# Optimization experiments

Hardware: AMD Instinct MI355X
Metric: run time of the kernel (lower is better)

Reference implementation:

```python
import jax, jax.numpy as jnp
import numpy as np

VOCAB, EMB, H, LAYERS, B, T = 50000, 128, 128, 3, 64, 512


def _lstm_dir(x, w_ih, w_hh, b_ih, b_hh, h0, c0, reverse):
    # x: [B,T,Din]; w_ih: [4H,Din]; w_hh: [4H,H]; h0,c0: [B,H]
    xg = jnp.einsum('btd,gd->btg', x, w_ih) + b_ih + b_hh  # [B,T,4H]

    def step(carry, xg_t):
        h, c = carry
        g = xg_t + h @ w_hh.T  # [B,4H]
        i, f, gg, o = jnp.split(g, 4, axis=-1)  # torch gate order i,f,g,o
        c = jax.nn.sigmoid(f) * c + jax.nn.sigmoid(i) * jnp.tanh(gg)
        h = jax.nn.sigmoid(o) * jnp.tanh(c)
        return (h, c), h

    _, hs = jax.lax.scan(step, (h0, c0), jnp.swapaxes(xg, 0, 1), reverse=reverse)
    return jnp.swapaxes(hs, 0, 1)  # [B,T,H], aligned with input time order


def _bidir_layer(x, w_ih, w_hh, b_ih, b_hh, h0, c0):
    # stacked params: leading dim 2 = (fwd, bwd)
    fwd = _lstm_dir(x, w_ih[0], w_hh[0], b_ih[0], b_hh[0], h0[0], c0[0], False)
    bwd = _lstm_dir(x, w_ih[1], w_hh[1], b_ih[1], b_hh[1], h0[1], c0[1], True)
    return jnp.concatenate([fwd, bwd], axis=-1)  # [B,T,2H]


def setup_inputs() -> dict:
    key = jax.random.key(0)
    ks = jax.random.split(key, 20)
    s = 1.0 / np.sqrt(H)
    inp = {
        'X_batch': jax.random.randint(ks[0], (B, T), 0, VOCAB),
        'emb': jax.random.normal(ks[1], (VOCAB, EMB), jnp.float32),
        'hx': jax.random.normal(ks[2], (2 * LAYERS, B, H), jnp.float32),
        'cx': jax.random.normal(ks[3], (2 * LAYERS, B, H), jnp.float32),
        'lin_w': jax.random.uniform(ks[4], (1, 2 * H), jnp.float32, -s, s),
        'lin_b': jax.random.uniform(ks[5], (1,), jnp.float32, -s, s),
    }
    k = 6
    for l in range(LAYERS):
        din = EMB if l == 0 else 2 * H
        inp[f'w_ih_{l}'] = jax.random.uniform(ks[k], (2, 4 * H, din), jnp.float32, -s, s); k += 1
        inp[f'w_hh_{l}'] = jax.random.uniform(ks[k], (2, 4 * H, H), jnp.float32, -s, s); k += 1
        inp[f'b_ih_{l}'] = jax.random.uniform(ks[k], (2, 4 * H), jnp.float32, -s, s); k += 1
        inp[f'b_hh_{l}'] = jax.random.uniform(ks[k], (2, 4 * H), jnp.float32, -s, s); k += 1
    return inp


def reference(X_batch, emb, hx, cx, lin_w, lin_b,
              w_ih_0, w_hh_0, b_ih_0, b_hh_0,
              w_ih_1, w_hh_1, b_ih_1, b_hh_1,
              w_ih_2, w_hh_2, b_ih_2, b_hh_2):
    x = emb[X_batch]  # [B,T,EMB]
    params = [(w_ih_0, w_hh_0, b_ih_0, b_hh_0),
              (w_ih_1, w_hh_1, b_ih_1, b_hh_1),
              (w_ih_2, w_hh_2, b_ih_2, b_hh_2)]
    for l, (wi, wh, bi, bh) in enumerate(params):
        x = _bidir_layer(x, wi, wh, bi, bh, hx[2 * l:2 * l + 2], cx[2 * l:2 * l + 2])
    # linear head applied to last timestep (== output[:, -1] of full linear)
    return x[:, -1] @ lin_w.T + lin_b  # [B,1]
```

## Files before the change

kernel.cpp:

```cpp
#include <hip/hip_runtime.h>
#include <hip/hip_bf16.h>
#include <stdint.h>

#define B_    64
#define T_    512
#define EMB_  128
#define H_    128
#define G4    512
#define M_    (B_ * T_)

typedef __attribute__((ext_vector_type(8))) short     short8;
typedef __attribute__((ext_vector_type(4))) float     floatx4;
typedef __attribute__((ext_vector_type(2))) _Float16  half2v;

#define GLDS(g, l) __builtin_amdgcn_global_load_lds( \
    (__attribute__((address_space(1))) void*)(g),    \
    (__attribute__((address_space(3))) void*)(l), 16, 0, 0)

__device__ __forceinline__ unsigned short f2bf_bits(float f) {
  __hip_bfloat16 h = __float2bfloat16(f);
  return *reinterpret_cast<unsigned short*>(&h);
}
__device__ __forceinline__ float bf_bits2f(unsigned short u) {
  unsigned int x = ((unsigned int)u) << 16;
  return __uint_as_float(x);
}
__device__ __forceinline__ float sigm(float x) {
  return __fdividef(1.0f, 1.0f + __expf(-x));
}
__device__ __forceinline__ float tanh_fast(float x) {
  return 1.0f - __fdividef(2.0f, __expf(2.0f * x) + 1.0f);
}

__device__ __forceinline__ unsigned int pack_f16x2(float a, float b) {
  half2v h; h.x = (_Float16)a; h.y = (_Float16)b;
  return __builtin_bit_cast(unsigned int, h);
}
__device__ __forceinline__ half2v u2h2(unsigned int u) {
  return __builtin_bit_cast(half2v, u);
}

#if __has_builtin(__builtin_amdgcn_fdot2)
__device__ __forceinline__ float fdot2(half2v a, half2v b, float c) {
  return __builtin_amdgcn_fdot2(a, b, c, false);
}
#else
__device__ __forceinline__ float fdot2(half2v a, half2v b, float c) {
  return fmaf((float)a.x, (float)b.x, fmaf((float)a.y, (float)b.y, c));
}
#endif

__device__ __forceinline__ float quad_sum(float x) {
  x += __int_as_float(
      __builtin_amdgcn_mov_dpp(__float_as_int(x), 0xB1, 0xF, 0xF, true));
  x += __int_as_float(
      __builtin_amdgcn_mov_dpp(__float_as_int(x), 0x4E, 0xF, 0xF, true));
  return x;
}

__device__ __forceinline__ void barrier_lds_only() {
  __builtin_amdgcn_s_waitcnt(0xC07F);
  __builtin_amdgcn_s_barrier();
}

__device__ __forceinline__ void  store_xg(float* p, float v)  { *p = v; }
__device__ __forceinline__ void  store_xg(unsigned short* p, float v) { *p = f2bf_bits(v); }
__device__ __forceinline__ float load_xg(const float* p)  { return *p; }
__device__ __forceinline__ float load_xg(const unsigned short* p) { return bf_bits2f(*p); }

__global__ void k_gather(const int* __restrict__ X, const float* __restrict__ emb,
                         unsigned short* __restrict__ x0) {
  int i = blockIdx.x * 256 + threadIdx.x;
  int row = i >> 5, c4 = i & 31;
  float4 v = ((const float4*)emb)[(size_t)X[row] * 32 + c4];
  ushort4 o;
  o.x = f2bf_bits(v.x); o.y = f2bf_bits(v.y); o.z = f2bf_bits(v.z); o.w = f2bf_bits(v.w);
  ((ushort4*)x0)[i] = o;
}

__global__ void k_prep(const float* __restrict__ w, const float* __restrict__ bi,
                       const float* __restrict__ bh, unsigned short* __restrict__ wb,
                       float* __restrict__ bias, int nw) {
  int i = blockIdx.x * blockDim.x + threadIdx.x;
  int stride = gridDim.x * blockDim.x;
  for (int k = i; k < nw; k += stride) wb[k] = f2bf_bits(w[k]);
  for (int k = i; k < 2 * G4; k += stride) bias[k] = bi[k] + bh[k];
}

__global__ void k_prep_whh(const float* __restrict__ Whh, unsigned int* __restrict__ wf) {
  int i = blockIdx.x * 256 + threadIdx.x;
  int dir   = i >> 15;
  int r     = i & 0x7FFF;
  int plane = r >> 9;
  int ts    = r & 511;
  int g = plane >> 4;
  int j = plane & 15;
  int l = ts & 63, w = ts >> 6;
  int p2 = l & 3, ul = l >> 2;
  int u  = w * 16 + ul;
  int k0 = 32 * p2 + 2 * j;
  const float* wr = Whh + ((size_t)dir * G4 + g * H_ + u) * H_ + k0;
  wf[i] = pack_f16x2(wr[0], wr[1]);
}

template <typename XG_T>
__global__ __launch_bounds__(256, 2) void k_gemm(
    const unsigned short* __restrict__ A,
    const unsigned short* __restrict__ W,
    const float* __restrict__ bias,
    XG_T* __restrict__ xg,
    int K) {
  __shared__ unsigned short sA[128 * 32];
  __shared__ unsigned short sB[128 * 32];
  const int tid  = threadIdx.x;
  const int lane = tid & 63;
  const int wave = tid >> 6;
  const int mt = blockIdx.x, nt = blockIdx.y, dir = blockIdx.z;
  const size_t Arow0 = (size_t)mt * 128;
  const int    Ncol0 = nt * 128;
  const unsigned short* Wd = W + (size_t)dir * G4 * K;

  const int srow = tid >> 2;
  const int qlog = (tid & 3) ^ ((tid >> 4) & 3);
  auto ldsA0 = (__attribute__((address_space(3))) void*)(sA + wave * 512);
  auto ldsA1 = (__attribute__((address_space(3))) void*)(sA + 2048 + wave * 512);
  auto ldsB0 = (__attribute__((address_space(3))) void*)(sB + wave * 512);
  auto ldsB1 = (__attribute__((address_space(3))) void*)(sB + 2048 + wave * 512);

  floatx4 acc[4][4];
#pragma unroll
  for (int i = 0; i < 4; ++i)
#pragma unroll
    for (int j = 0; j < 4; ++j) acc[i][j] = (floatx4)0.0f;

  const int wrow = (wave >> 1) * 64, wcol = (wave & 1) * 64;
  const int frow = lane & 15;
  const int fq   = lane >> 4;

  for (int kt = 0; kt < K; kt += 32) {
    const unsigned short* gA0 = A  + (Arow0 + srow) * (size_t)K + kt + qlog * 8;
    const unsigned short* gB0 = Wd + (size_t)(Ncol0 + srow) * K + kt + qlog * 8;
    GLDS(gA0, ldsA0);
    GLDS(gA0 + (size_t)64 * K, ldsA1);
    GLDS(gB0, ldsB0);
    GLDS(gB0 + (size_t)64 * K, ldsB1);
    __syncthreads();

    short8 af[4], bf[4];
#pragma unroll
    for (int i = 0; i < 4; ++i) {
      int r  = wrow + 16 * i + frow;
      int rn = wcol + 16 * i + frow;
      af[i] = *(const short8*)(sA + r  * 32 + ((fq ^ ((r  >> 2) & 3)) * 8));
      bf[i] = *(const short8*)(sB + rn * 32 + ((fq ^ ((rn >> 2) & 3)) * 8));
    }
#pragma unroll
    for (int i = 0; i < 4; ++i)
#pragma unroll
      for (int j = 0; j < 4; ++j)
        acc[i][j] = __builtin_amdgcn_mfma_f32_16x16x32_bf16(af[i], bf[j], acc[i][j], 0, 0, 0);
    __syncthreads();
  }

  const int r0 = (lane >> 4) * 4;
  const int cc = lane & 15;
  XG_T* xgd = xg + (size_t)dir * M_ * G4;
#pragma unroll
  for (int j = 0; j < 4; ++j) {
    int gcol = Ncol0 + wcol + 16 * j + cc;
    float bs = bias[dir * G4 + gcol];
#pragma unroll
    for (int i = 0; i < 4; ++i) {
      size_t rowb = Arow0 + wrow + 16 * i + r0;
#pragma unroll
      for (int r = 0; r < 4; ++r)
        store_xg(&xgd[(rowb + r) * G4 + gcol], acc[i][j][r] + bs);
    }
  }
}

template <typename XG_T>
__global__ __attribute__((amdgpu_flat_work_group_size(512, 512),
                          amdgpu_waves_per_eu(2, 2))) void k_scan(
    const unsigned int* __restrict__ wf,
    const float* __restrict__ hx0,
    const float* __restrict__ cx0,
    const XG_T* __restrict__ xg,
    unsigned short* __restrict__ y)
{
  const int b   = blockIdx.x & 63;
  const int dir = blockIdx.x >> 6;
  const int tid = threadIdx.x;
  const int lane = tid & 63;
  const int wave = tid >> 6;
  const int p2 = lane & 3;
  const int ul = lane >> 2;
  const int u  = wave * 16 + ul;

  __shared__ __align__(16) unsigned short h16[2][128];

  unsigned int wvs[64];
#pragma unroll
  for (int i = 0; i < 64; ++i) wvs[i] = wf[((dir * 64 + i) << 9) + tid];

  float c = cx0[(size_t)dir * B_ * H_ + b * H_ + u];
  if (p2 == 0) {
    float h0 = hx0[(size_t)dir * B_ * H_ + b * H_ + u];
    h16[0][u] = (unsigned short)(pack_f16x2(h0, 0.0f) & 0xFFFF);
  }

  const XG_T* xgb = xg + ((size_t)dir * M_ + (size_t)b * T_) * G4;
  const intptr_t xstep = dir ? -(intptr_t)G4 : (intptr_t)G4;
  const int o0 = p2 * H_ + u;
  const XG_T* xrow0 = xgb + (dir ? (size_t)(T_ - 1) * G4 : 0);
  float xa0 = load_xg(xrow0 + o0);
  float xa1 = load_xg(xrow0 + xstep + o0);
  const XG_T* xld = xrow0 + 2 * xstep;

  unsigned short* yp = y + ((size_t)b * T_ + (dir ? T_ - 1 : 0)) * (2 * H_)
                         + dir * H_ + u;
  const intptr_t ystep = dir ? -(intptr_t)(2 * H_) : (intptr_t)(2 * H_);

  __syncthreads();

  auto step = [&](int par, float xv) {
    const char* hb = (const char*)&h16[par][0] + 64 * p2;
    uint4 hq[4];
#pragma unroll
    for (int i = 0; i < 4; ++i) hq[i] = *(const uint4*)(hb + 16 * i);
    unsigned int hhd[16];
#pragma unroll
    for (int i = 0; i < 4; ++i) {
      hhd[4 * i + 0] = hq[i].x; hhd[4 * i + 1] = hq[i].y;
      hhd[4 * i + 2] = hq[i].z; hhd[4 * i + 3] = hq[i].w;
    }
    float A0 = (p2 == 0) ? xv : 0.0f, B0 = 0;
    float A1 = (p2 == 1) ? xv : 0.0f, B1 = 0;
    float A2 = (p2 == 2) ? xv : 0.0f, B2 = 0;
    float A3 = (p2 == 3) ? xv : 0.0f, B3 = 0;
#pragma unroll
    for (int j = 0; j < 8; ++j) {
      int j1 = j + 8;
      A0 = fdot2(u2h2(wvs[0 * 16 + j]),  u2h2(hhd[j]),  A0);
      A1 = fdot2(u2h2(wvs[1 * 16 + j]),  u2h2(hhd[j]),  A1);
      A2 = fdot2(u2h2(wvs[2 * 16 + j]),  u2h2(hhd[j]),  A2);
      A3 = fdot2(u2h2(wvs[3 * 16 + j]),  u2h2(hhd[j]),  A3);
      B0 = fdot2(u2h2(wvs[0 * 16 + j1]), u2h2(hhd[j1]), B0);
      B1 = fdot2(u2h2(wvs[1 * 16 + j1]), u2h2(hhd[j1]), B1);
      B2 = fdot2(u2h2(wvs[2 * 16 + j1]), u2h2(hhd[j1]), B2);
      B3 = fdot2(u2h2(wvs[3 * 16 + j1]), u2h2(hhd[j1]), B3);
    }
    float g0 = quad_sum(A0 + B0);
    float g1 = quad_sum(A1 + B1);
    float g2 = quad_sum(A2 + B2);
    float g3 = quad_sum(A3 + B3);
    float iv = sigm(g0), fv = sigm(g1), gv = tanh_fast(g2), ov = sigm(g3);
    c = fmaf(fv, c, iv * gv);
    float h = ov * tanh_fast(c);
    if (p2 == 0) {
      h16[par ^ 1][u] = (unsigned short)(pack_f16x2(h, 0.0f) & 0xFFFF);
      *yp = f2bf_bits(h);
    }
    yp += ystep;
    barrier_lds_only();
  };

  for (int t = 0; t < T_; t += 2) {
    {
      float xv = xa0;
      xa0 = load_xg(xld + o0);
      xld += xstep;
      step(0, xv);
    }
    {
      float xv = xa1;
      xa1 = load_xg(xld + o0);
      xld += xstep;
      step(1, xv);
    }
  }
}

__global__ void k_head(const unsigned short* __restrict__ y2, const float* __restrict__ lw,
                       const float* __restrict__ lb, float* __restrict__ out) {
  int b = blockIdx.x, l = threadIdx.x;
  const unsigned short* row = y2 + ((size_t)b * T_ + (T_ - 1)) * (2 * H_);
  float s = 0;
#pragma unroll
  for (int k = 0; k < 4; ++k) s += bf_bits2f(row[l + 64 * k]) * lw[l + 64 * k];
#pragma unroll
  for (int off = 32; off > 0; off >>= 1) s += __shfl_down(s, off);
  if (l == 0) out[b] = s + lb[0];
}

template <typename XG_T>
static inline void run_layers(const unsigned int* const* wfs,
                              const unsigned short* x0,
                              unsigned short* y0, unsigned short* y1, unsigned short* y2,
                              const unsigned short* wb0, const unsigned short* wb1,
                              const unsigned short* wb2,
                              const float* bias0, const float* bias1, const float* bias2,
                              const float* hx, const float* cx,
                              XG_T* xg, hipStream_t stream) {
  dim3 gg(M_ / 128, G4 / 128, 2);
  k_gemm<XG_T><<<gg, 256, 0, stream>>>(x0, wb0, bias0, xg, EMB_);
  k_scan<XG_T><<<128, 512, 0, stream>>>(wfs[0], hx, cx, xg, y0);
  k_gemm<XG_T><<<gg, 256, 0, stream>>>(y0, wb1, bias1, xg, 2 * H_);
  k_scan<XG_T><<<128, 512, 0, stream>>>(wfs[1], hx + 2 * B_ * H_, cx + 2 * B_ * H_, xg, y1);
  k_gemm<XG_T><<<gg, 256, 0, stream>>>(y1, wb2, bias2, xg, 2 * H_);
  k_scan<XG_T><<<128, 512, 0, stream>>>(wfs[2], hx + 4 * B_ * H_, cx + 4 * B_ * H_, xg, y2);
}

extern "C" void kernel_launch(void* const* d_in, const int* in_sizes, int n_in,
                              void* d_out, int out_size, void* d_ws, size_t ws_size,
                              hipStream_t stream) {
  const int*   X   = (const int*)d_in[0];
  const float* emb = (const float*)d_in[1];
  const float* hx  = (const float*)d_in[2];
  const float* cx  = (const float*)d_in[3];
  const float* lw  = (const float*)d_in[4];
  const float* lb  = (const float*)d_in[5];
  const float* w_ih[3] = {(const float*)d_in[6],  (const float*)d_in[10], (const float*)d_in[14]};
  const float* w_hh[3] = {(const float*)d_in[7],  (const float*)d_in[11], (const float*)d_in[15]};
  const float* b_ih[3] = {(const float*)d_in[8],  (const float*)d_in[12], (const float*)d_in[16]};
  const float* b_hh[3] = {(const float*)d_in[9],  (const float*)d_in[13], (const float*)d_in[17]};
  float* out = (float*)d_out;

  char* ws = (char*)d_ws;
  size_t off = 0;
  auto carve = [&](size_t bytes) {
    char* p = ws + off;
    off = (off + bytes + 255) & ~(size_t)255;
    return p;
  };
  unsigned short* x0  = (unsigned short*)carve((size_t)M_ * EMB_ * 2);
  unsigned short* y0  = (unsigned short*)carve((size_t)M_ * 2 * H_ * 2);
  unsigned short* y1  = (unsigned short*)carve((size_t)M_ * 2 * H_ * 2);
  unsigned short* y2  = (unsigned short*)carve((size_t)M_ * 2 * H_ * 2);
  unsigned short* wb0 = (unsigned short*)carve((size_t)2 * G4 * EMB_ * 2);
  unsigned short* wb1 = (unsigned short*)carve((size_t)2 * G4 * 2 * H_ * 2);
  unsigned short* wb2 = (unsigned short*)carve((size_t)2 * G4 * 2 * H_ * 2);
  float* bias0 = (float*)carve(2 * G4 * 4);
  float* bias1 = (float*)carve(2 * G4 * 4);
  float* bias2 = (float*)carve(2 * G4 * 4);
  unsigned int* wf0 = (unsigned int*)carve((size_t)65536 * 4);
  unsigned int* wf1 = (unsigned int*)carve((size_t)65536 * 4);
  unsigned int* wf2 = (unsigned int*)carve((size_t)65536 * 4);
  const size_t xg_f32_bytes = (size_t)2 * M_ * G4 * 4;
  const bool use_f32 = (off + xg_f32_bytes) <= ws_size;
  void* xg = carve(use_f32 ? xg_f32_bytes : xg_f32_bytes / 2);

  k_prep<<<256, 256, 0, stream>>>(w_ih[0], b_ih[0], b_hh[0], wb0, bias0, 2 * G4 * EMB_);
  k_prep<<<256, 256, 0, stream>>>(w_ih[1], b_ih[1], b_hh[1], wb1, bias1, 2 * G4 * 2 * H_);
  k_prep<<<256, 256, 0, stream>>>(w_ih[2], b_ih[2], b_hh[2], wb2, bias2, 2 * G4 * 2 * H_);
  k_prep_whh<<<256, 256, 0, stream>>>(w_hh[0], wf0);
  k_prep_whh<<<256, 256, 0, stream>>>(w_hh[1], wf1);
  k_prep_whh<<<256, 256, 0, stream>>>(w_hh[2], wf2);
  k_gather<<<(M_ * 32) / 256, 256, 0, stream>>>(X, emb, x0);

  const unsigned int* wfs[3] = {wf0, wf1, wf2};
  if (use_f32)
    run_layers<float>(wfs, x0, y0, y1, y2, wb0, wb1, wb2, bias0, bias1, bias2,
                      hx, cx, (float*)xg, stream);
  else
    run_layers<unsigned short>(wfs, x0, y0, y1, y2, wb0, wb1, wb2, bias0, bias1, bias2,
                               hx, cx, (unsigned short*)xg, stream);

  k_head<<<64, 64, 0, stream>>>(y2, lw, lb, out);
}
```

Before: 1.370 ms.

## Compute LSTM recurrent matvec with MFMA instead of fdot2 in scan kernel

Replaces the per-step fdot2-based recurrent matvec (512 threads, quad DPP reduction) with 16x16x32 f16 MFMA instructions over 256 threads. Each wave holds W_hh fragments as MFMA B operands, and only row 0 of the A operand carries h, so 15 of 16 rows are wasted. The W_hh prep layout is rewritten to match. The aim is to cut the serial per-step latency of the recurrence by dropping the dot-product chain and cross-lane reductions, at the cost of MFMA latency and wasted matrix rows.

```diff
diff --git a/kernel.cpp b/kernel.cpp
--- a/kernel.cpp
+++ b/kernel.cpp
@@ -12,6 +12,7 @@
 typedef __attribute__((ext_vector_type(8))) short     short8;
 typedef __attribute__((ext_vector_type(4))) float     floatx4;
 typedef __attribute__((ext_vector_type(2))) _Float16  half2v;
+typedef __attribute__((ext_vector_type(8))) _Float16  half8;
 
 #define GLDS(g, l) __builtin_amdgcn_global_load_lds( \
     (__attribute__((address_space(1))) void*)(g),    \
@@ -31,31 +32,9 @@
 __device__ __forceinline__ float tanh_fast(float x) {
   return 1.0f - __fdividef(2.0f, __expf(2.0f * x) + 1.0f);
 }
-
 __device__ __forceinline__ unsigned int pack_f16x2(float a, float b) {
   half2v h; h.x = (_Float16)a; h.y = (_Float16)b;
   return __builtin_bit_cast(unsigned int, h);
-}
-__device__ __forceinline__ half2v u2h2(unsigned int u) {
-  return __builtin_bit_cast(half2v, u);
-}
-
-#if __has_builtin(__builtin_amdgcn_fdot2)
-__device__ __forceinline__ float fdot2(half2v a, half2v b, float c) {
-  return __builtin_amdgcn_fdot2(a, b, c, false);
-}
-#else
-__device__ __forceinline__ float fdot2(half2v a, half2v b, float c) {
-  return fmaf((float)a.x, (float)b.x, fmaf((float)a.y, (float)b.y, c));
-}
-#endif
-
-__device__ __forceinline__ float quad_sum(float x) {
-  x += __int_as_float(
-      __builtin_amdgcn_mov_dpp(__float_as_int(x), 0xB1, 0xF, 0xF, true));
-  x += __int_as_float(
-      __builtin_amdgcn_mov_dpp(__float_as_int(x), 0x4E, 0xF, 0xF, true));
-  return x;
 }
 
 __device__ __forceinline__ void barrier_lds_only() {
@@ -89,17 +68,17 @@
 
 __global__ void k_prep_whh(const float* __restrict__ Whh, unsigned int* __restrict__ wf) {
   int i = blockIdx.x * 256 + threadIdx.x;
-  int dir   = i >> 15;
-  int r     = i & 0x7FFF;
-  int plane = r >> 9;
-  int ts    = r & 511;
-  int g = plane >> 4;
-  int j = plane & 15;
-  int l = ts & 63, w = ts >> 6;
-  int p2 = l & 3, ul = l >> 2;
-  int u  = w * 16 + ul;
-  int k0 = 32 * p2 + 2 * j;
-  const float* wr = Whh + ((size_t)dir * G4 + g * H_ + u) * H_ + k0;
+  int jp  = i & 3;
+  int l   = (i >> 2) & 63;
+  int kk  = (i >> 8) & 3;
+  int uh  = (i >> 10) & 1;
+  int g   = (i >> 11) & 3;
+  int w   = (i >> 13) & 3;
+  int dir = (i >> 15) & 1;
+  int u   = w * 32 + uh * 16 + (l & 15);
+  int row = g * 128 + u;
+  int k0  = kk * 32 + (l >> 4) * 8 + 2 * jp;
+  const float* wr = Whh + ((size_t)dir * G4 + row) * H_ + k0;
   wf[i] = pack_f16x2(wr[0], wr[1]);
 }
 
@@ -180,8 +159,8 @@
 }
 
 template <typename XG_T>
-__global__ __attribute__((amdgpu_flat_work_group_size(512, 512),
-                          amdgpu_waves_per_eu(2, 2))) void k_scan(
+__global__ __attribute__((amdgpu_flat_work_group_size(256, 256),
+                          amdgpu_waves_per_eu(1, 1))) void k_scan(
     const unsigned int* __restrict__ wf,
     const float* __restrict__ hx0,
     const float* __restrict__ cx0,
@@ -192,92 +171,119 @@
   const int dir = blockIdx.x >> 6;
   const int tid = threadIdx.x;
   const int lane = tid & 63;
-  const int wave = tid >> 6;
-  const int p2 = lane & 3;
-  const int ul = lane >> 2;
-  const int u  = wave * 16 + ul;
+  const int w    = tid >> 6;
+  const int l15  = lane & 15;
+  const int seg  = lane >> 4;
+  const bool row0 = (l15 == 0);
 
   __shared__ __align__(16) unsigned short h16[2][128];
 
-  unsigned int wvs[64];
-#pragma unroll
-  for (int i = 0; i < 64; ++i) wvs[i] = wf[((dir * 64 + i) << 9) + tid];
-
-  float c = cx0[(size_t)dir * B_ * H_ + b * H_ + u];
-  if (p2 == 0) {
-    float h0 = hx0[(size_t)dir * B_ * H_ + b * H_ + u];
-    h16[0][u] = (unsigned short)(pack_f16x2(h0, 0.0f) & 0xFFFF);
-  }
+  half8 wB[4][2][4];
+  {
+    const uint4* wv4 = (const uint4*)wf;
+#pragma unroll
+    for (int g = 0; g < 4; ++g)
+#pragma unroll
+      for (int uh = 0; uh < 2; ++uh)
+#pragma unroll
+        for (int kk = 0; kk < 4; ++kk) {
+          int idx = ((((dir * 4 + w) * 4 + g) * 2 + uh) * 4 + kk) * 64 + lane;
+          wB[g][uh][kk] = __builtin_bit_cast(half8, wv4[idx]);
+        }
+  }
+
+  float c[2];
+#pragma unroll
+  for (int uh = 0; uh < 2; ++uh)
+    c[uh] = cx0[(size_t)dir * B_ * H_ + b * H_ + (w * 32 + uh * 16 + l15)];
+
+  if (tid < 128) {
+    float h0 = hx0[(size_t)dir * B_ * H_ + b * H_ + tid];
+    h16[0][tid] = (unsigned short)(pack_f16x2(h0, 0.0f) & 0xFFFF);
+  }
+
+  floatx4 acc[4][2];
+#pragma unroll
+  for (int g = 0; g < 4; ++g)
+#pragma unroll
+    for (int uh = 0; uh < 2; ++uh) acc[g][uh] = (floatx4)0.0f;
 
   const XG_T* xgb = xg + ((size_t)dir * M_ + (size_t)b * T_) * G4;
   const intptr_t xstep = dir ? -(intptr_t)G4 : (intptr_t)G4;
-  const int o0 = p2 * H_ + u;
+  int xofs[4][2];
+#pragma unroll
+  for (int g = 0; g < 4; ++g)
+#pragma unroll
+    for (int uh = 0; uh < 2; ++uh)
+      xofs[g][uh] = g * H_ + w * 32 + uh * 16 + l15;
   const XG_T* xrow0 = xgb + (dir ? (size_t)(T_ - 1) * G4 : 0);
-  float xa0 = load_xg(xrow0 + o0);
-  float xa1 = load_xg(xrow0 + xstep + o0);
+  float xpA[4][2], xpB[4][2];
+#pragma unroll
+  for (int g = 0; g < 4; ++g)
+#pragma unroll
+    for (int uh = 0; uh < 2; ++uh) {
+      xpA[g][uh] = load_xg(xrow0 + xofs[g][uh]);
+      xpB[g][uh] = load_xg(xrow0 + xstep + xofs[g][uh]);
+    }
   const XG_T* xld = xrow0 + 2 * xstep;
 
   unsigned short* yp = y + ((size_t)b * T_ + (dir ? T_ - 1 : 0)) * (2 * H_)
-                         + dir * H_ + u;
+                         + dir * H_;
   const intptr_t ystep = dir ? -(intptr_t)(2 * H_) : (intptr_t)(2 * H_);
 
   __syncthreads();
 
-  auto step = [&](int par, float xv) {
-    const char* hb = (const char*)&h16[par][0] + 64 * p2;
-    uint4 hq[4];
-#pragma unroll
-    for (int i = 0; i < 4; ++i) hq[i] = *(const uint4*)(hb + 16 * i);
-    unsigned int hhd[16];
-#pragma unroll
-    for (int i = 0; i < 4; ++i) {
-      hhd[4 * i + 0] = hq[i].x; hhd[4 * i + 1] = hq[i].y;
-      hhd[4 * i + 2] = hq[i].z; hhd[4 * i + 3] = hq[i].w;
-    }
-    float A0 = (p2 == 0) ? xv : 0.0f, B0 = 0;
-    float A1 = (p2 == 1) ? xv : 0.0f, B1 = 0;
-    float A2 = (p2 == 2) ? xv : 0.0f, B2 = 0;
-    float A3 = (p2 == 3) ? xv : 0.0f, B3 = 0;
-#pragma unroll
-    for (int j = 0; j < 8; ++j) {
-      int j1 = j + 8;
-      A0 = fdot2(u2h2(wvs[0 * 16 + j]),  u2h2(hhd[j]),  A0);
-      A1 = fdot2(u2h2(wvs[1 * 16 + j]),  u2h2(hhd[j]),  A1);
-      A2 = fdot2(u2h2(wvs[2 * 16 + j]),  u2h2(hhd[j]),  A2);
-      A3 = fdot2(u2h2(wvs[3 * 16 + j]),  u2h2(hhd[j]),  A3);
-      B0 = fdot2(u2h2(wvs[0 * 16 + j1]), u2h2(hhd[j1]), B0);
-      B1 = fdot2(u2h2(wvs[1 * 16 + j1]), u2h2(hhd[j1]), B1);
-      B2 = fdot2(u2h2(wvs[2 * 16 + j1]), u2h2(hhd[j1]), B2);
-      B3 = fdot2(u2h2(wvs[3 * 16 + j1]), u2h2(hhd[j1]), B3);
-    }
-    float g0 = quad_sum(A0 + B0);
-    float g1 = quad_sum(A1 + B1);
-    float g2 = quad_sum(A2 + B2);
-    float g3 = quad_sum(A3 + B3);
-    float iv = sigm(g0), fv = sigm(g1), gv = tanh_fast(g2), ov = sigm(g3);
-    c = fmaf(fv, c, iv * gv);
-    float h = ov * tanh_fast(c);
-    if (p2 == 0) {
-      h16[par ^ 1][u] = (unsigned short)(pack_f16x2(h, 0.0f) & 0xFFFF);
-      *yp = f2bf_bits(h);
+  auto step = [&](int par, float (&xp)[4][2]) {
+    half8 af[4];
+#pragma unroll
+    for (int kk = 0; kk < 4; ++kk) {
+      uint4 hv = *(const uint4*)((const char*)&h16[par][0] + kk * 64 + seg * 16);
+      uint4 av;
+      av.x = row0 ? hv.x : 0u; av.y = row0 ? hv.y : 0u;
+      av.z = row0 ? hv.z : 0u; av.w = row0 ? hv.w : 0u;
+      af[kk] = __builtin_bit_cast(half8, av);
+    }
+
+#pragma unroll
+    for (int g = 0; g < 4; ++g)
+#pragma unroll
+      for (int uh = 0; uh < 2; ++uh) {
+        acc[g][uh][0] = xp[g][uh];
+        xp[g][uh] = load_xg(xld + xofs[g][uh]);
+      }
+    xld += xstep;
+
+#pragma unroll
+    for (int kk = 0; kk < 4; ++kk)
+#pragma unroll
+      for (int g = 0; g < 4; ++g)
+#pragma unroll
+        for (int uh = 0; uh < 2; ++uh)
+          acc[g][uh] = __builtin_amdgcn_mfma_f32_16x16x32_f16(
+              af[kk], wB[g][uh][kk], acc[g][uh], 0, 0, 0);
+
+#pragma unroll
+    for (int uh = 0; uh < 2; ++uh) {
+      float gi = acc[0][uh][0];
+      float gf = acc[1][uh][0];
+      float gg = acc[2][uh][0];
+      float go = acc[3][uh][0];
+      float iv = sigm(gi), fv = sigm(gf), gv = tanh_fast(gg), ov = sigm(go);
+      c[uh] = fmaf(fv, c[uh], iv * gv);
+      float h = ov * tanh_fast(c[uh]);
+      if (lane < 16) {
+        int u = w * 32 + uh * 16 + l15;
+        h16[par ^ 1][u] = (unsigned short)(pack_f16x2(h, 0.0f) & 0xFFFF);
+        yp[u] = f2bf_bits(h);
+      }
     }
     yp += ystep;
     barrier_lds_only();
   };
 
   for (int t = 0; t < T_; t += 2) {
-    {
-      float xv = xa0;
-      xa0 = load_xg(xld + o0);
-      xld += xstep;
-      step(0, xv);
-    }
-    {
-      float xv = xa1;
-      xa1 = load_xg(xld + o0);
-      xld += xstep;
-      step(1, xv);
-    }
+    step(0, xpA);
+    step(1, xpB);
   }
 }
 
@@ -304,11 +310,11 @@
                               XG_T* xg, hipStream_t stream) {
   dim3 gg(M_ / 128, G4 / 128, 2);
   k_gemm<XG_T><<<gg, 256, 0, stream>>>(x0, wb0, bias0, xg, EMB_);
-  k_scan<XG_T><<<128, 512, 0, stream>>>(wfs[0], hx, cx, xg, y0);
+  k_scan<XG_T><<<128, 256, 0, stream>>>(wfs[0], hx, cx, xg, y0);
   k_gemm<XG_T><<<gg, 256, 0, stream>>>(y0, wb1, bias1, xg, 2 * H_);
-  k_scan<XG_T><<<128, 512, 0, stream>>>(wfs[1], hx + 2 * B_ * H_, cx + 2 * B_ * H_, xg, y1);
+  k_scan<XG_T><<<128, 256, 0, stream>>>(wfs[1], hx + 2 * B_ * H_, cx + 2 * B_ * H_, xg, y1);
   k_gemm<XG_T><<<gg, 256, 0, stream>>>(y1, wb2, bias2, xg, 2 * H_);
-  k_scan<XG_T><<<128, 512, 0, stream>>>(wfs[2], hx + 4 * B_ * H_, cx + 4 * B_ * H_, xg, y2);
+  k_scan<XG_T><<<128, 256, 0, stream>>>(wfs[2], hx + 4 * B_ * H_, cx + 4 * B_ * H_, xg, y2);
 }
 
 extern "C" void kernel_launch(void* const* d_in, const int* in_sizes, int n_in,
```

Result: slower. 1.521 ms (+11.1%).
